# Performance work log

Measured on AMD Instinct MI355X. Metric: run time of the kernel, lower is better.

## Reference

```python
import jax, jax.numpy as jnp
import numpy as np

B, S, D, L = 8, 512, 768, 200


def leaky(x, slope=0.2):
    return jnp.where(x >= 0, x, slope * x)


def l1_normalize(x, axis):
    # torch.nn.functional.normalize(p=1): x / max(sum|x|, 1e-12)
    return x / jnp.maximum(jnp.sum(jnp.abs(x), axis=axis, keepdims=True), 1e-12)


def setup_inputs() -> dict:
    key = jax.random.key(0)
    ks = jax.random.split(key, 16)
    s = 1.0 / np.sqrt(D)
    return {
        "doc_embedding": jax.random.normal(ks[0], (B, S, D), jnp.float32),
        "labels": jax.random.uniform(ks[1], (B, L), jnp.float32),
        "label_embed": jax.random.normal(ks[2], (L, D), jnp.float32),
        "label_adj": jax.random.uniform(ks[3], (L, L), jnp.float32),
        "w_gcn3": jax.random.uniform(ks[4], (D, D), jnp.float32, -s, s),
        "w_gcn5": jax.random.uniform(ks[5], (D, D), jnp.float32, -s, s),
        "w_ll1": jax.random.normal(ks[6], (D, D), jnp.float32) * s,
        "b_ll1": jax.random.normal(ks[7], (D,), jnp.float32) * s,
        "w_ll2": jax.random.normal(ks[8], (D, D), jnp.float32) * s,
        "b_ll2": jax.random.normal(ks[9], (D,), jnp.float32) * s,
        "w_lin": jax.random.normal(ks[10], (2 * D, D), jnp.float32) * (1.0 / np.sqrt(2 * D)),
        "b_lin": jax.random.normal(ks[11], (D,), jnp.float32) * s,
        "conv_w": jax.random.normal(ks[12], (L, 1, 9, 9), jnp.float32) * (1.0 / 9.0),
        "conv_b": jax.random.normal(ks[13], (L,), jnp.float32) * 0.01,
        "w_lin1": jax.random.normal(ks[14], (D, L), jnp.float32) * s,
        "b_lin1": jax.random.normal(ks[15], (L,), jnp.float32) * s,
    }


def reference(doc_embedding, labels, label_embed, label_adj, w_gcn3, w_gcn5,
              w_ll1, b_ll1, w_ll2, b_ll2, w_lin, b_lin, conv_w, conv_b,
              w_lin1, b_lin1):
    b = doc_embedding.shape[0]
    # stacked (replicated) label embeddings: [B, L, D]
    le = jnp.broadcast_to(label_embed, (b,) + label_embed.shape)

    # GCN3: adj @ (x @ W), leaky relu 0.2
    le = leaky(jnp.einsum('lm,bmd->bld', label_adj, le @ w_gcn3))

    # learned adjacency A = sigmoid(lin1(le) @ lin2(le)^T)   [B, L, L]
    q = le @ w_ll1 + b_ll1
    k = le @ w_ll2 + b_ll2
    A = jax.nn.sigmoid(jnp.einsum('bld,bmd->blm', q, k))

    # normalize_adj: D^{-1/2} with detached row sum; out = (A D)^T D
    row_sum = jax.lax.stop_gradient(jnp.sum(A, axis=1))  # [B, L]
    d_inv_sqrt = jnp.where(row_sum > 0, row_sum ** -0.5, 0.0)
    AD = A * d_inv_sqrt[:, None, :]                 # A @ diag(d)
    A_norm = jnp.swapaxes(AD, 1, 2) * d_inv_sqrt[:, None, :]

    # GCN5 with learned adj
    d_le = leaky(jnp.einsum('blm,bmd->bld', A_norm, le @ w_gcn5))

    le_cat = jnp.concatenate([le, d_le], axis=-1)   # [B, L, 2D]
    le_out = le_cat @ w_lin + b_lin                 # [B, L, D]

    le_out = l1_normalize(le_out, axis=-2)
    doc = l1_normalize(doc_embedding, axis=-2)

    # word-label attention map [B, S, L]
    wla = jnp.einsum('bsd,bld->bsl', doc, le_out)

    # conv2d 1 -> L channels, 9x9, pad 4 over [B, 1, S, L]
    att = jax.lax.conv_general_dilated(
        wla[:, None, :, :], conv_w, window_strides=(1, 1),
        padding=((4, 4), (4, 4)),
        dimension_numbers=('NCHW', 'OIHW', 'NCHW'))
    att = att + conv_b[None, :, None, None]         # [B, L, S, L]

    att = jnp.max(att, axis=1)                      # [B, S, L]
    att = jnp.max(att, axis=-1, keepdims=True)      # [B, S, 1]
    gate = jnp.tanh(att)

    h_enc = jnp.sum(gate * doc, axis=1)             # [B, D]
    label_output = jax.nn.sigmoid(h_enc @ w_lin1 + b_lin1)

    eps = 1e-7
    p = jnp.clip(label_output, eps, 1.0 - eps)
    loss = -jnp.mean(labels * jnp.log(p) + (1.0 - labels) * jnp.log(1.0 - p))
    return label_output, loss
```

## Files before the change

kernel.cpp:

```cpp
#include <hip/hip_runtime.h>
#include <hip/hip_bf16.h>
#include <math.h>

#define BB 8
#define SS 512
#define DD 768
#define LL 200

typedef __attribute__((ext_vector_type(8))) short bf16x8;
typedef __attribute__((ext_vector_type(4))) float f32x4;

__device__ inline short f2bf(float f) {
    unsigned u = __builtin_bit_cast(unsigned, f);
    unsigned r = (u + 0x7FFFu + ((u >> 16) & 1u)) >> 16;
    return (short)r;
}
__device__ inline float bf2f(short s) {
    unsigned u = ((unsigned)(unsigned short)s) << 16;
    return __builtin_bit_cast(float, u);
}

#define LDP3 264
#define BK3  256
#define MGLDS (2 * 64 * LDP3 * 2)

template<int EPI, bool TB>
__global__ __launch_bounds__(256, 1) void mgemm_k(
    const short* __restrict__ A, int lda,
    const void* __restrict__ Bv, int ldb,
    const float* __restrict__ bias,
    const void* __restrict__ Bv2, const float* __restrict__ bias2, int nsplit,
    const void* __restrict__ Bv3, const float* __restrict__ bias3, int nsplit2,
    float* __restrict__ Cf, int ldc,
    short* __restrict__ Cb, int ldcb,
    short* __restrict__ Ct, int ldct, int nsplitT,
    int M, int N, int K)
{
    extern __shared__ short dsm[];
    short* As = dsm;
    short* Bs = dsm + 64 * LDP3;
    const int tid = threadIdx.x;
    const int bm = blockIdx.y * 64;
    const int bn = blockIdx.x * 64;
    int bnb = bn;
    if (!TB) {
        if (bn >= nsplit2)      { Bv = Bv3; bias = bias3; bnb = bn - nsplit2; }
        else if (bn >= nsplit)  { Bv = Bv2; bias = bias2; bnb = bn - nsplit; }
    }
    const int w = tid >> 6, lane = tid & 63, g = lane >> 4, ln = lane & 15;
    const int Kp = (K + BK3 - 1) & ~(BK3 - 1);
    const int nt = Kp >> 8;

    const int ar = tid >> 2, ac = tid & 3;
    const int bn_ = tid & 63, bko = (tid >> 6) * 64;

    f32x4 acc[4];
    #pragma unroll
    for (int i = 0; i < 4; ++i) acc[i] = (f32x4){0.f, 0.f, 0.f, 0.f};

    bf16x8 aR[8], bT[8];
    #pragma unroll
    for (int j = 0; j < 8; ++j) { aR[j] = (bf16x8){0,0,0,0,0,0,0,0}; bT[j] = (bf16x8){0,0,0,0,0,0,0,0}; }
    float bF[64];
    #pragma unroll
    for (int j = 0; j < 64; ++j) bF[j] = 0.f;

    const int gmS = bm + ar;
    const bool aOk = (gmS < M);

    auto fetchA = [&](int k0) {
        if (aOk) {
            const short* p = A + (size_t)gmS * lda + k0 + ac * 64;
            #pragma unroll
            for (int j = 0; j < 8; ++j) aR[j] = *(const bf16x8*)(p + j * 8);
        }
    };
    auto fetchB = [&](int k0) {
        if (TB) {
            const short* Bt = (const short*)Bv;
            int gn = bn + ar;
            if (gn < N) {
                const short* p = Bt + (size_t)gn * ldb + k0 + ac * 64;
                #pragma unroll
                for (int j = 0; j < 8; ++j) bT[j] = *(const bf16x8*)(p + j * 8);
            }
        } else {
            const float* Bp = (const float*)Bv + (size_t)(bnb + bn_);
            #pragma unroll
            for (int j = 0; j < 64; ++j) {
                int gk = k0 + bko + j;
                bF[j] = (gk < K) ? Bp[(size_t)gk * ldb] : 0.f;
            }
        }
    };

    fetchA(0);
    fetchB(0);

    for (int t = 0; t < nt; ++t) {
        {
            short* pa = As + ar * LDP3 + ac * 64;
            #pragma unroll
            for (int j = 0; j < 8; ++j) *(bf16x8*)(pa + j * 8) = aR[j];
        }
        if (TB) {
            short* pb = Bs + ar * LDP3 + ac * 64;
            #pragma unroll
            for (int j = 0; j < 8; ++j) *(bf16x8*)(pb + j * 8) = bT[j];
        } else {
            short* pb = Bs + bn_ * LDP3 + bko;
            #pragma unroll
            for (int q = 0; q < 8; ++q) {
                bf16x8 v;
                #pragma unroll
                for (int e = 0; e < 8; ++e) v[e] = f2bf(bF[q * 8 + e]);
                *(bf16x8*)(pb + q * 8) = v;
            }
        }
        __syncthreads();

        if (t + 1 < nt) {
            int k0 = (t + 1) << 8;
            fetchA(k0);
            fetchB(k0);
        }

        #pragma unroll
        for (int ks = 0; ks < 8; ++ks) {
            bf16x8 a = *(const bf16x8*)(As + (w * 16 + ln) * LDP3 + ks * 32 + g * 8);
            #pragma unroll
            for (int nb = 0; nb < 4; ++nb) {
                bf16x8 b = *(const bf16x8*)(Bs + (nb * 16 + ln) * LDP3 + ks * 32 + g * 8);
                acc[nb] = __builtin_amdgcn_mfma_f32_16x16x32_bf16(a, b, acc[nb], 0, 0, 0);
            }
        }
        __syncthreads();
    }

    #pragma unroll
    for (int nb = 0; nb < 4; ++nb) {
        int gn = bn + nb * 16 + ln;
        float bv = (bias && gn < N) ? bias[bnb + nb * 16 + ln] : 0.f;
        #pragma unroll
        for (int r = 0; r < 4; ++r) {
            int gm = bm + w * 16 + g * 4 + r;
            if (gm < M && gn < N) {
                float v = acc[nb][r] + bv;
                if (EPI == 1) v = (v >= 0.f) ? v : 0.2f * v;
                else if (EPI == 2) v = 1.f / (1.f + expf(-v));
                if (Cf) Cf[(size_t)gm * ldc + gn] = v;
                if (Cb) Cb[(size_t)gm * ldcb + gn] = f2bf(v);
                if (Ct && gn >= nsplitT)
                    Ct[(size_t)(gn - nsplitT) * ldct + gm] = f2bf(v);
            }
        }
    }
}

#define WP 168
#define TP 24
#define WTR 217
#define WROWS 208
#define APAD 256
#define BIGN (1 << 30)

__global__ void prep2_k(const float* __restrict__ cw, const float* __restrict__ cb,
                        const float* __restrict__ adj, const float* __restrict__ doc,
                        short* __restrict__ wkg, short* __restrict__ adj_bf,
                        short* __restrict__ docb)
{
    if (blockIdx.x < 96) {
        int u = blockIdx.x;
        int dc = u % 12, b = u / 12;
        int dx = threadIdx.x & 63, sy = threadIdx.x >> 6;
        int d = dc * 64 + dx;
        const float* pp = doc + (size_t)b * SS * DD + d;
        float s = 0.f;
        for (int t = sy; t < SS; t += 4) s += fabsf(pp[(size_t)t * DD]);
        __shared__ float red[4][64];
        red[sy][dx] = s;
        __syncthreads();
        float dn = fmaxf(red[0][dx] + red[1][dx] + red[2][dx] + red[3][dx], 1e-12f);
        float inv = 1.f / dn;
        short* qq = docb + (size_t)b * SS * DD + d;
        for (int t = sy; t < SS; t += 4) qq[(size_t)t * DD] = f2bf(pp[(size_t)t * DD] * inv);
        return;
    }
    int idx = (blockIdx.x - 96) * 256 + threadIdx.x;
    if (idx < WROWS * WP) {
        int o = idx / WP, kk = idx % WP;
        int kj = kk >> 4, ki = kk & 15;
        float v = 0.f;
        if (o < LL && kj < 9) {
            if (ki < 9) v = cw[o * 81 + ki * 9 + kj];
            else if (ki == 9 && kj == 0) v = cb[o];
        }
        wkg[idx] = f2bf(v);
        return;
    }
    idx -= WROWS * WP;
    if (idx < LL * APAD) {
        int r = idx / APAD, c = idx % APAD;
        adj_bf[idx] = f2bf(c < LL ? adj[r * LL + c] : 0.f);
    }
}

__global__ void ca_k(const float* __restrict__ A, short* __restrict__ An)
{
    int i = blockIdx.x;
    int j = threadIdx.x;
    float si = 0.f, sj = 0.f;
    for (int l = 0; l < LL; ++l) {
        si += A[l * LL + i];
        if (j < LL) sj += A[l * LL + j];
    }
    float di = (si > 0.f) ? (1.f / sqrtf(si)) : 0.f;
    float dj = (sj > 0.f) ? (1.f / sqrtf(sj)) : 0.f;
    float v = (j < LL) ? A[j * LL + i] * di * dj : 0.f;
    An[i * APAD + j] = f2bf(v);
}

__global__ void l1n_k(const float* __restrict__ X, short* __restrict__ Xb)
{
    int c = threadIdx.x >> 5, r = threadIdx.x & 31;
    int col = blockIdx.x * 8 + c;
    float s = 0.f;
    for (int l = r; l < LL; l += 32) s += fabsf(X[l * DD + col]);
    #pragma unroll
    for (int off = 16; off > 0; off >>= 1) s += __shfl_xor(s, off, 64);
    float inv = 1.f / fmaxf(s, 1e-12f);
    for (int l = r; l < LL; l += 32)
        Xb[l * DD + col] = f2bf(X[l * DD + col] * inv);
}

__global__ __launch_bounds__(512, 1) void conv_max_k(
    const float* __restrict__ wla,
    const short* __restrict__ wkg,
    float* __restrict__ gate)
{
    extern __shared__ short smem[];
    short* Wk   = smem;
    short* winT = Wk + WROWS * WP;
    short* wbf  = winT + 4 * WTR * TP;
    __shared__ float wredf[8];

    const int blk = blockIdx.x;
    const int b = blk >> 7;
    const int s0 = (blk & 127) << 2;
    const int tid = threadIdx.x;

    {
        const int4* src = (const int4*)wkg;
        int4* dst = (int4*)Wk;
        for (int i = tid; i < WROWS * WP / 8; i += 512) dst[i] = src[i];
    }
    for (int idx = tid; idx < 12 * 216; idx += 512) {
        int r = idx / 216, c = idx % 216;
        int sr = s0 - 4 + r, col = c - 4;
        float v = 0.f;
        if (sr >= 0 && sr < SS && col >= 0 && col < LL)
            v = wla[((size_t)b * SS + sr) * LL + col];
        wbf[idx] = f2bf(v);
    }
    __syncthreads();
    for (int idx = tid; idx < 4 * WTR; idx += 512) {
        int p = idx / WTR, r = idx % WTR;
        short vals[16];
        #pragma unroll
        for (int i = 0; i < 9; ++i) vals[i] = (r < 216) ? wbf[(p + i) * 216 + r] : (short)0;
        vals[9] = (short)0x3F80;
        #pragma unroll
        for (int i = 10; i < 16; ++i) vals[i] = 0;
        short* dstp = winT + (p * WTR + r) * TP;
        *(bf16x8*)dstp = *(const bf16x8*)vals;
        *(bf16x8*)(dstp + 8) = *(const bf16x8*)(vals + 8);
    }
    __syncthreads();

    const int w = tid >> 6;
    const int p = w >> 1;
    const int h = w & 1;
    const int lane = tid & 63;
    const int g = lane >> 4;
    const int ln = lane & 15;
    const short* WT = winT + p * WTR * TP;

    bf16x8 Af[7][5];
    #pragma unroll
    for (int s = 0; s < 7; ++s) {
        int st = h * 7 + s;
        if (st > 12) st = 12;
        #pragma unroll
        for (int j = 0; j < 5; ++j)
            Af[s][j] = *(const bf16x8*)(Wk + (st * 16 + ln) * WP + j * 32 + g * 8);
    }

    float lm = -INFINITY;

    auto loadB = [&](int nt, bf16x8 (&Bf)[5]) {
        #pragma unroll
        for (int j = 0; j < 5; ++j)
            Bf[j] = *(const bf16x8*)(WT + (nt * 16 + ln + 2 * j + (g >> 1)) * TP + (g & 1) * 8);
    };
    auto compute = [&](int nt, const bf16x8 (&Bf)[5]) {
        #pragma unroll
        for (int s = 0; s < 7; ++s) {
            if (h == 0 || s < 6) {
                int st = h * 7 + s;
                f32x4 acc = {0.f, 0.f, 0.f, 0.f};
                #pragma unroll
                for (int j = 0; j < 5; ++j)
                    acc = __builtin_amdgcn_mfma_f32_16x16x32_bf16(Af[s][j], Bf[j], acc, 0, 0, 0);
                float t = fmaxf(fmaxf(acc[0], acc[1]), fmaxf(acc[2], acc[3]));
                bool ok = (st < 12 || g < 2) && (nt < 12 || ln < 8);
                lm = ok ? fmaxf(lm, t) : lm;
            }
        }
    };

    bf16x8 B0[5], B1[5];
    loadB(0, B0);
    for (int nt = 0; nt < 12; nt += 2) {
        loadB(nt + 1, B1);
        compute(nt, B0);
        loadB(nt + 2, B0);
        compute(nt + 1, B1);
    }
    compute(12, B0);

    #pragma unroll
    for (int off = 32; off > 0; off >>= 1)
        lm = fmaxf(lm, __shfl_xor(lm, off, 64));
    if (lane == 0) wredf[w] = lm;
    __syncthreads();
    if (tid < 4)
        gate[((size_t)b << 9) + s0 + tid] = tanhf(fmaxf(wredf[2 * tid], wredf[2 * tid + 1]));
}

__global__ void henc_part_k(const short* __restrict__ doc_nb, const float* __restrict__ gate,
                            float* __restrict__ hpart)
{
    int dc = blockIdx.x, sc = blockIdx.y, b = blockIdx.z;
    int dx = threadIdx.x & 63, sy = threadIdx.x >> 6;
    int d = dc * 64 + dx;
    float s = 0.f;
    for (int t = sy; t < 64; t += 4) {
        int srow = sc * 64 + t;
        s = fmaf(bf2f(doc_nb[((size_t)b * SS + srow) * DD + d]), gate[b * SS + srow], s);
    }
    __shared__ float red[4][64];
    red[sy][dx] = s;
    __syncthreads();
    if (sy == 0)
        hpart[((size_t)b * 8 + sc) * DD + d] = red[0][dx] + red[1][dx] + red[2][dx] + red[3][dx];
}

__global__ void final2_k(const float* __restrict__ hpart,
                         const float* __restrict__ W, const float* __restrict__ bias,
                         float* __restrict__ out)
{
    int b = blockIdx.x, tid = threadIdx.x;
    __shared__ float hb[DD];
    for (int idx = tid; idx < DD; idx += 256) {
        float s = 0.f;
        #pragma unroll
        for (int sc = 0; sc < 8; ++sc) s += hpart[((size_t)b * 8 + sc) * DD + idx];
        hb[idx] = s;
    }
    __syncthreads();
    int l = tid;
    if (l < LL) {
        float acc = bias[l];
        for (int d = 0; d < DD; ++d) acc = fmaf(hb[d], W[d * LL + l], acc);
        out[b * LL + l] = 1.f / (1.f + expf(-acc));
    }
}

__global__ void loss_k(const float* __restrict__ out, const float* __restrict__ labels,
                       float* __restrict__ loss_out)
{
    float s = 0.f;
    for (int i = threadIdx.x; i < BB * LL; i += 256) {
        float p = out[i];
        p = fminf(fmaxf(p, 1e-7f), 1.f - 1e-7f);
        float y = labels[i];
        s += y * logf(p) + (1.f - y) * logf(1.f - p);
    }
    #pragma unroll
    for (int off = 32; off > 0; off >>= 1) s += __shfl_down(s, off, 64);
    __shared__ float ws[4];
    if ((threadIdx.x & 63) == 0) ws[threadIdx.x >> 6] = s;
    __syncthreads();
    if (threadIdx.x == 0)
        loss_out[0] = -(ws[0] + ws[1] + ws[2] + ws[3]) / (float)(BB * LL);
}

static void mgemm(hipStream_t st, int epi, bool tb,
                  const short* A, int lda, const void* B, int ldb,
                  const float* bias,
                  const void* B2, const float* bias2, int nsplit,
                  const void* B3, const float* bias3, int nsplit2,
                  float* Cf, int ldc, short* Cb, int ldcb,
                  short* Ct, int ldct, int nsplitT,
                  int M, int N, int K)
{
    dim3 g((N + 63) / 64, (M + 63) / 64);
    #define LAUNCH(E, T) do { \
        (void)hipFuncSetAttribute((const void*)mgemm_k<E, T>, \
                                  hipFuncAttributeMaxDynamicSharedMemorySize, MGLDS); \
        mgemm_k<E, T><<<g, 256, MGLDS, st>>>(A, lda, B, ldb, bias, B2, bias2, nsplit, \
                                             B3, bias3, nsplit2, Cf, ldc, Cb, ldcb, \
                                             Ct, ldct, nsplitT, M, N, K); \
    } while (0)
    if (!tb) {
        if (epi == 0)      LAUNCH(0, false);
        else if (epi == 1) LAUNCH(1, false);
        else               LAUNCH(2, false);
    } else {
        if (epi == 0)      LAUNCH(0, true);
        else if (epi == 1) LAUNCH(1, true);
        else               LAUNCH(2, true);
    }
    #undef LAUNCH
}

extern "C" void kernel_launch(void* const* d_in, const int* in_sizes, int n_in,
                              void* d_out, int out_size, void* d_ws, size_t ws_size,
                              hipStream_t stream)
{
    const float* doc_emb   = (const float*)d_in[0];
    const float* labels    = (const float*)d_in[1];
    const float* label_emb = (const float*)d_in[2];
    const float* label_adj = (const float*)d_in[3];
    const float* w_gcn3    = (const float*)d_in[4];
    const float* w_gcn5    = (const float*)d_in[5];
    const float* w_ll1     = (const float*)d_in[6];
    const float* b_ll1     = (const float*)d_in[7];
    const float* w_ll2     = (const float*)d_in[8];
    const float* b_ll2     = (const float*)d_in[9];
    const float* w_lin     = (const float*)d_in[10];
    const float* b_lin     = (const float*)d_in[11];
    const float* conv_w    = (const float*)d_in[12];
    const float* conv_b    = (const float*)d_in[13];
    const float* w_lin1    = (const float*)d_in[14];
    const float* b_lin1    = (const float*)d_in[15];

    float* out = (float*)d_out;

    char* p = (char*)d_ws;
    auto alloc = [&](size_t bytes) { void* r = p; p += (bytes + 15) & ~(size_t)15; return r; };
    short* wkg       = (short*)alloc(WROWS * WP * 2);
    short* adj_bf    = (short*)alloc(200 * APAD * 2);
    short* E2_bf     = (short*)alloc(200 * 768 * 2);
    short* le_cat_bf = (short*)alloc(200 * 1536 * 2);
    short* qkh_bf    = (short*)alloc(200 * 2304 * 2);
    short* Ht        = (short*)alloc(768 * 256 * 2);
    float* Amat      = (float*)alloc(200 * 200 * 4);
    short* Anorm_bf  = (short*)alloc(200 * APAD * 2);
    float* le_out_f  = (float*)alloc(200 * 768 * 4);
    short* le_out_bf = (short*)alloc(200 * 768 * 2);
    short* doc_nb    = (short*)alloc((size_t)BB * SS * DD * 2);
    float* wla       = (float*)alloc((size_t)BB * SS * LL * 4);
    float* gatev     = (float*)alloc(BB * SS * 4);
    float* hpart     = (float*)alloc(BB * 8 * DD * 4);

    prep2_k<<<96 + (WROWS * WP + LL * APAD + 255) / 256, 256, 0, stream>>>(
        conv_w, conv_b, label_adj, doc_emb, wkg, adj_bf, doc_nb);
    mgemm(stream, 0, false, adj_bf, APAD, label_emb, DD, nullptr,
          nullptr, nullptr, BIGN, nullptr, nullptr, BIGN,
          nullptr, 0, E2_bf, DD, nullptr, 0, BIGN, LL, DD, LL);
    mgemm(stream, 1, false, E2_bf, DD, w_gcn3, DD, nullptr,
          nullptr, nullptr, BIGN, nullptr, nullptr, BIGN,
          nullptr, 0, le_cat_bf, 1536, nullptr, 0, BIGN, LL, DD, DD);
    mgemm(stream, 0, false, le_cat_bf, 1536, w_ll1, DD, b_ll1,
          w_ll2, b_ll2, DD, w_gcn5, nullptr, 2 * DD,
          nullptr, 0, qkh_bf, 2304, Ht, 256, 2 * DD, LL, 3 * DD, DD);
    mgemm(stream, 2, true, qkh_bf, 2304, qkh_bf + DD, 2304, nullptr,
          nullptr, nullptr, BIGN, nullptr, nullptr, BIGN,
          Amat, LL, nullptr, 0, nullptr, 0, BIGN, LL, LL, DD);
    ca_k<<<LL, 256, 0, stream>>>(Amat, Anorm_bf);
    mgemm(stream, 1, true, Anorm_bf, APAD, Ht, 256, nullptr,
          nullptr, nullptr, BIGN, nullptr, nullptr, BIGN,
          nullptr, 0, le_cat_bf + DD, 1536, nullptr, 0, BIGN, LL, DD, LL);
    mgemm(stream, 0, false, le_cat_bf, 1536, w_lin, DD, b_lin,
          nullptr, nullptr, BIGN, nullptr, nullptr, BIGN,
          le_out_f, DD, nullptr, 0, nullptr, 0, BIGN, LL, DD, 2 * DD);
    l1n_k<<<96, 256, 0, stream>>>(le_out_f, le_out_bf);
    mgemm(stream, 0, true, doc_nb, DD, le_out_bf, DD, nullptr,
          nullptr, nullptr, BIGN, nullptr, nullptr, BIGN,
          wla, LL, nullptr, 0, nullptr, 0, BIGN, BB * SS, LL, DD);
    (void)hipFuncSetAttribute((const void*)conv_max_k,
                              hipFuncAttributeMaxDynamicSharedMemorySize, 116736);
    conv_max_k<<<1024, 512, 116736, stream>>>(wla, wkg, gatev);
    henc_part_k<<<dim3(12, 8, 8), 256, 0, stream>>>(doc_nb, gatev, hpart);
    final2_k<<<BB, 256, 0, stream>>>(hpart, w_lin1, b_lin1, out);
    loss_k<<<1, 256, 0, stream>>>(out, labels, out + BB * LL);
}
```

Measured before the change: 306.7 us.

## Split doc L1-normalize into partial-sum and vectorized normalize kernels

The doc-embedding column L1 normalization used to run in only 96 blocks, each looping over all 512 rows with scalar strided accesses. It is now two kernels. The first computes per-chunk partial column sums over a 12x8x8 grid. The second reads float4s across the whole tensor, adds up the eight partials and writes bf16 output with short4 stores. This exposes far more parallelism for a memory-bound pass, at the cost of two extra launches, a small workspace buffer and a second read of doc.

```diff
diff --git a/kernel.cpp b/kernel.cpp
--- a/kernel.cpp
+++ b/kernel.cpp
@@ -164,29 +164,11 @@
 #define APAD 256
 #define BIGN (1 << 30)
 
-__global__ void prep2_k(const float* __restrict__ cw, const float* __restrict__ cb,
-                        const float* __restrict__ adj, const float* __restrict__ doc,
-                        short* __restrict__ wkg, short* __restrict__ adj_bf,
-                        short* __restrict__ docb)
-{
-    if (blockIdx.x < 96) {
-        int u = blockIdx.x;
-        int dc = u % 12, b = u / 12;
-        int dx = threadIdx.x & 63, sy = threadIdx.x >> 6;
-        int d = dc * 64 + dx;
-        const float* pp = doc + (size_t)b * SS * DD + d;
-        float s = 0.f;
-        for (int t = sy; t < SS; t += 4) s += fabsf(pp[(size_t)t * DD]);
-        __shared__ float red[4][64];
-        red[sy][dx] = s;
-        __syncthreads();
-        float dn = fmaxf(red[0][dx] + red[1][dx] + red[2][dx] + red[3][dx], 1e-12f);
-        float inv = 1.f / dn;
-        short* qq = docb + (size_t)b * SS * DD + d;
-        for (int t = sy; t < SS; t += 4) qq[(size_t)t * DD] = f2bf(pp[(size_t)t * DD] * inv);
-        return;
-    }
-    int idx = (blockIdx.x - 96) * 256 + threadIdx.x;
+__global__ void prep_k(const float* __restrict__ cw, const float* __restrict__ cb,
+                       const float* __restrict__ adj,
+                       short* __restrict__ wkg, short* __restrict__ adj_bf)
+{
+    int idx = blockIdx.x * blockDim.x + threadIdx.x;
     if (idx < WROWS * WP) {
         int o = idx / WP, kk = idx % WP;
         int kj = kk >> 4, ki = kk & 15;
@@ -231,6 +213,46 @@
     float inv = 1.f / fmaxf(s, 1e-12f);
     for (int l = r; l < LL; l += 32)
         Xb[l * DD + col] = f2bf(X[l * DD + col] * inv);
+}
+
+__global__ void docsumA_k(const float* __restrict__ doc, float* __restrict__ dpart)
+{
+    int dc = blockIdx.x, sc = blockIdx.y, b = blockIdx.z;
+    int dx = threadIdx.x & 63, sy = threadIdx.x >> 6;
+    int d = dc * 64 + dx;
+    const float* pp = doc + ((size_t)b * SS + sc * 64) * DD + d;
+    float s = 0.f;
+    for (int t = sy; t < 64; t += 4) s += fabsf(pp[(size_t)t * DD]);
+    __shared__ float red[4][64];
+    red[sy][dx] = s;
+    __syncthreads();
+    if (sy == 0)
+        dpart[((size_t)b * 8 + sc) * DD + d] = red[0][dx] + red[1][dx] + red[2][dx] + red[3][dx];
+}
+
+__global__ void docbfB_k(const float* __restrict__ doc, const float* __restrict__ dpart,
+                         short* __restrict__ docb)
+{
+    int gid = blockIdx.x * blockDim.x + threadIdx.x;
+    if (gid >= BB * SS * DD / 4) return;
+    size_t base = (size_t)gid * 4;
+    int d = (int)(base % DD);
+    int b = (int)(base / ((size_t)SS * DD));
+    float4 v = *(const float4*)(doc + base);
+    float4 dn = {0.f, 0.f, 0.f, 0.f};
+    #pragma unroll
+    for (int sc = 0; sc < 8; ++sc) {
+        float4 t = *(const float4*)(dpart + ((size_t)b * 8 + sc) * DD + d);
+        dn.x += t.x; dn.y += t.y; dn.z += t.z; dn.w += t.w;
+    }
+    dn.x = fmaxf(dn.x, 1e-12f); dn.y = fmaxf(dn.y, 1e-12f);
+    dn.z = fmaxf(dn.z, 1e-12f); dn.w = fmaxf(dn.w, 1e-12f);
+    short4 o;
+    o.x = f2bf(v.x / dn.x);
+    o.y = f2bf(v.y / dn.y);
+    o.z = f2bf(v.z / dn.z);
+    o.w = f2bf(v.w / dn.w);
+    *(short4*)(docb + base) = o;
 }
 
 __global__ __launch_bounds__(512, 1) void conv_max_k(
@@ -459,13 +481,16 @@
     short* Anorm_bf  = (short*)alloc(200 * APAD * 2);
     float* le_out_f  = (float*)alloc(200 * 768 * 4);
     short* le_out_bf = (short*)alloc(200 * 768 * 2);
+    float* dpart     = (float*)alloc(BB * 8 * DD * 4);
     short* doc_nb    = (short*)alloc((size_t)BB * SS * DD * 2);
     float* wla       = (float*)alloc((size_t)BB * SS * LL * 4);
     float* gatev     = (float*)alloc(BB * SS * 4);
     float* hpart     = (float*)alloc(BB * 8 * DD * 4);
 
-    prep2_k<<<96 + (WROWS * WP + LL * APAD + 255) / 256, 256, 0, stream>>>(
-        conv_w, conv_b, label_adj, doc_emb, wkg, adj_bf, doc_nb);
+    docsumA_k<<<dim3(12, 8, 8), 256, 0, stream>>>(doc_emb, dpart);
+    docbfB_k<<<(BB * SS * DD / 4 + 255) / 256, 256, 0, stream>>>(doc_emb, dpart, doc_nb);
+    prep_k<<<(WROWS * WP + LL * APAD + 255) / 256, 256, 0, stream>>>(
+        conv_w, conv_b, label_adj, wkg, adj_bf);
     mgemm(stream, 0, false, adj_bf, APAD, label_emb, DD, nullptr,
           nullptr, nullptr, BIGN, nullptr, nullptr, BIGN,
           nullptr, 0, E2_bf, DD, nullptr, 0, BIGN, LL, DD, LL);
```

New measurement: 277.4 us. -9.5%, faster.
